# Kernel tuning notes

Hardware: AMD Instinct MI355X
Metric: run time of the kernel (lower is better)

## Reference

```python
import jax, jax.numpy as jnp
import numpy as np
from jax import lax

K = 5        # kernel_size
KN = 32      # kernel_num
C_IN = 16
PRIOR_VAR = 0.01


def _extract_patches(x, k):
    # TF tf.image.extract_patches VALID, stride 1: last-dim order is (kh, kw, c)
    B, H, W, C = x.shape
    Ho, Wo = H - k + 1, W - k + 1
    p = jnp.stack([x[:, i:i + Ho, j:j + Wo, :] for i in range(k) for j in range(k)], axis=3)
    return p.reshape(B, Ho * Wo, k * k * C)  # [B, P, k*k*C]


def setup_inputs() -> dict:
    key = jax.random.key(0)
    k1, k2, k3, k4 = jax.random.split(key, 4)
    mu_in = jax.random.normal(k1, (32, 64, 64, C_IN), dtype=jnp.float32)
    Sigma_in = jax.random.uniform(k2, (32, 64, 64, C_IN), dtype=jnp.float32)
    # GlorotNormal for w_mu
    fan_in = K * K * C_IN
    fan_out = K * K * KN
    std = jnp.sqrt(2.0 / (fan_in + fan_out)).astype(jnp.float32)
    w_mu = jax.random.normal(k3, (K, K, C_IN, KN), dtype=jnp.float32) * std
    w_sigma = jax.random.uniform(k4, (KN,), dtype=jnp.float32, minval=-4.6, maxval=-2.25)
    return {"mu_in": mu_in, "Sigma_in": Sigma_in, "w_mu": w_mu, "w_sigma": w_sigma}


def reference(mu_in, Sigma_in, w_mu, w_sigma):
    B = mu_in.shape[0]
    # KL regularizer (broadcast w_sigma over w_mu shape, mean over all)
    kl_loss = (jnp.log(PRIOR_VAR) - 1.0 - w_sigma
               + jax.nn.softplus(w_sigma) / PRIOR_VAR
               + jnp.square(w_mu) / PRIOR_VAR)
    kl_conv = 0.5 * jnp.mean(kl_loss)

    w_sigma_2 = jax.nn.softplus(w_sigma)  # [KN]

    # mean path: standard conv
    mu_out = lax.conv_general_dilated(
        mu_in, w_mu, window_strides=(1, 1), padding='VALID',
        dimension_numbers=('NHWC', 'HWIO', 'NHWC'))  # [B, Ho, Wo, KN]
    Ho = mu_out.shape[1]

    mu_dim = jnp.float32(K * K * C_IN)

    diag_sigma_g = _extract_patches(Sigma_in, K)          # [B, P, D]
    mu_in_patches = _extract_patches(mu_in, K)            # [B, P, D]

    mu_cov_square = jnp.square(w_mu).reshape(K * K * C_IN, KN)
    mu_wT_sigmags_mu_w = diag_sigma_g @ (mu_cov_square / mu_dim)          # [B, P, KN]
    trace = jnp.sum(diag_sigma_g, axis=2, keepdims=True) * w_sigma_2 / mu_dim  # [B, P, KN]
    mu_gT_mu_g = jnp.sum(jnp.square(mu_in_patches), axis=-1, keepdims=True)    # [B, P, 1]
    sigmaw_mu_gT_mu_g = mu_gT_mu_g * w_sigma_2 / mu_dim                   # [B, P, KN]

    Sigma_out = trace + mu_wT_sigmags_mu_w + sigmaw_mu_gT_mu_g
    Sigma_out = jax.nn.softplus(Sigma_out.reshape(B, Ho, Ho, KN))
    return mu_out, Sigma_out, kl_conv
```

## Files before the change

kernel.cpp:

```cpp
#include <hip/hip_runtime.h>
#include <hip/hip_bf16.h>
#include <math.h>

#define KK 5
#define KN 32
#define CIN 16
#define H 64
#define W 64
#define NB 32
#define HO 60
#define WO 60
#define D_TOT 400
#define OUT_PLANE (NB*HO*WO*KN)

#define TH 8
#define TW 16
#define IN_R 12
#define IN_C 20
#define CPAD 24
#define TILE_SH (IN_R*IN_C*CPAD)
#define NPOS 25

typedef short short8 __attribute__((ext_vector_type(8)));
typedef float f32x16 __attribute__((ext_vector_type(16)));

__device__ ushort g_bmu[NPOS * 64 * 8];
__device__ ushort g_bsq[NPOS * 64 * 8];
__device__ float  g_spw[KN];

__device__ __forceinline__ ushort f2bf(float x) {
    __hip_bfloat16 h = __float2bfloat16(x);
    return *reinterpret_cast<ushort*>(&h);
}
__device__ __forceinline__ float softplusf(float x) {
    return (x > 20.0f) ? x : __logf(1.0f + __expf(x));
}

__global__ void prep_all(const float* __restrict__ w_mu, const float* __restrict__ w_sigma,
                         float* __restrict__ kl_out) {
    __shared__ float red[256];
    int t = threadIdx.x;
    if (blockIdx.x < 50) {
        int idx = blockIdx.x * 256 + t;
        int j  = idx & 7;
        int l  = (idx >> 3) & 63;
        int ts = idx >> 9;
        int cin = ((l >> 5) & 1) * 8 + j;
        int n   = l & 31;
        float w = w_mu[ts * 512 + cin * 32 + n];
        g_bmu[idx] = f2bf(w);
        g_bsq[idx] = f2bf(w * w * (1.0f / 400.0f));
    } else {
        float s = 0.f;
        for (int i = t; i < D_TOT * KN; i += 256) { float w = w_mu[i]; s += w * w; }
        red[t] = s;
        __syncthreads();
        for (int off = 128; off > 0; off >>= 1) {
            if (t < off) red[t] += red[t + off];
            __syncthreads();
        }
        float sum_w2 = red[0];
        if (t < KN) {
            float ws = w_sigma[t];
            g_spw[t] = log1pf(expf(ws)) * (1.0f / 400.0f);
        }
        if (t == 0) {
            float sws = 0.f;
            for (int kn = 0; kn < KN; ++kn) {
                float ws = w_sigma[kn];
                float sp = log1pf(expf(ws));
                sws += -ws + sp * 100.0f;
            }
            float kl = 0.5f * (-4.605170186f - 1.0f + sws * (1.0f / 32.0f)
                               + sum_w2 * (100.0f / 12800.0f));
            *kl_out = kl;
        }
    }
}

__global__ __launch_bounds__(256, 4)
void vdp_main(const float* __restrict__ mu_in, const float* __restrict__ sig_in,
              float* __restrict__ mu_out, float* __restrict__ sig_out) {
    __shared__ ushort tiles[2 * TILE_SH];
    __shared__ float csum[IN_R * IN_C];
    __shared__ float t12s[TH * TW];

    const int b   = blockIdx.z;
    const int ho0 = blockIdx.y * TH;
    const int wo0 = blockIdx.x * TW;
    const int t   = threadIdx.x;

    for (int i = t; i < IN_R * IN_C * 4; i += 256) {
        int pix = i >> 2, c4 = i & 3;
        int row = pix / IN_C;
        int col = pix - row * IN_C;
        int gh = ho0 + row, gw = wo0 + col;
        float4 vm = make_float4(0.f, 0.f, 0.f, 0.f), vs = vm;
        if (gh < H && gw < W) {
            size_t g = (((size_t)b * H + gh) * W + gw) * CIN + c4 * 4;
            vm = *(const float4*)(mu_in + g);
            vs = *(const float4*)(sig_in + g);
        }
        int sb = pix * CPAD + c4 * 4;
        ushort4 um, us;
        um.x = f2bf(vm.x); um.y = f2bf(vm.y); um.z = f2bf(vm.z); um.w = f2bf(vm.w);
        us.x = f2bf(vs.x); us.y = f2bf(vs.y); us.z = f2bf(vs.z); us.w = f2bf(vs.w);
        *(ushort4*)&tiles[sb] = um;
        *(ushort4*)&tiles[TILE_SH + sb] = us;
        float part = vs.x + vs.y + vs.z + vs.w
                   + vm.x * vm.x + vm.y * vm.y + vm.z * vm.z + vm.w * vm.w;
        part += __shfl_down(part, 2, 4);
        part += __shfl_down(part, 1, 4);
        if (c4 == 0) csum[pix] = part;
    }
    __syncthreads();

    if (t < TH * TW) {
        int r = t >> 4, c = t & 15;
        float s = 0.f;
#pragma unroll
        for (int kh = 0; kh < KK; ++kh)
#pragma unroll
            for (int kw = 0; kw < KK; ++kw)
                s += csum[(r + kh) * IN_C + c + kw];
        t12s[t] = s;
    }
    __syncthreads();

    const int w   = t >> 6;
    const int l   = t & 63;
    const int p   = l & 31;
    const int hi  = l >> 5;
    const int pr  = p >> 4;
    const int pc  = p & 15;

    const char* lds = (const char*)tiles;
    const int abase = ((2 * w + pr) * IN_C + pc) * (CPAD * 2) + hi * 16;

    const short8* Bmu8 = (const short8*)g_bmu;
    const short8* Bsq8 = (const short8*)g_bsq;

    f32x16 accm = {0.f}, accs = {0.f};
#pragma unroll
    for (int kh = 0; kh < KK; ++kh) {
#pragma unroll
        for (int kw = 0; kw < KK; ++kw) {
            const int ts  = kh * KK + kw;
            const int off = (kh * IN_C + kw) * (CPAD * 2);
            short8 am = *(const short8*)(lds + abase + off);
            short8 as = *(const short8*)(lds + abase + off + TILE_SH * 2);
            short8 bm = Bmu8[ts * 64 + l];
            short8 bs = Bsq8[ts * 64 + l];
            accm = __builtin_amdgcn_mfma_f32_32x32x16_bf16(am, bm, accm, 0, 0, 0);
            accs = __builtin_amdgcn_mfma_f32_32x32x16_bf16(as, bs, accs, 0, 0, 0);
        }
    }

    const int n = l & 31;
    const float spwn = g_spw[n];
#pragma unroll
    for (int reg = 0; reg < 16; ++reg) {
        int rloc = (reg & 3) + 8 * (reg >> 2) + 4 * hi;
        int lr = rloc >> 4, lc = rloc & 15;
        int ho = ho0 + 2 * w + lr;
        int wo = wo0 + lc;
        if (ho < HO && wo < WO) {
            float t12v = t12s[(2 * w + lr) * TW + lc];
            size_t base = (((size_t)b * HO + ho) * WO + wo) * KN + n;
            mu_out[base]  = accm[reg];
            sig_out[base] = softplusf(accs[reg] + t12v * spwn);
        }
    }
}

extern "C" void kernel_launch(void* const* d_in, const int* in_sizes, int n_in,
                              void* d_out, int out_size, void* d_ws, size_t ws_size,
                              hipStream_t stream) {
    const float* mu_in   = (const float*)d_in[0];
    const float* sig_in  = (const float*)d_in[1];
    const float* w_mu    = (const float*)d_in[2];
    const float* w_sigma = (const float*)d_in[3];

    float* out     = (float*)d_out;
    float* mu_out  = out;
    float* sig_out = out + (size_t)OUT_PLANE;
    float* kl_out  = out + 2 * (size_t)OUT_PLANE;

    (void)d_ws; (void)ws_size;

    prep_all<<<51, 256, 0, stream>>>(w_mu, w_sigma, kl_out);
    vdp_main<<<dim3(4, 8, NB), 256, 0, stream>>>(mu_in, sig_in, mu_out, sig_out);
}
```

Baseline: 114.1 us.

## Fuse weight prep into main kernel using atomic tickets and spin-wait

Merges the weight-preparation kernel into the main conv kernel. The first 26 blocks to draw an atomic ticket build the bf16 weight fragments and the KL term, and every block spin-waits on a done counter before its MFMA loop. The per-channel softplus scale now lives in shared memory. This removes one kernel launch and the gap between launches, at the cost of a global spin barrier and counters that the last block must reset. It relies on the ticketed blocks being resident, and concurrent launches could race on the shared counters.

```diff
diff --git a/kernel.cpp b/kernel.cpp
--- a/kernel.cpp
+++ b/kernel.cpp
@@ -20,13 +20,16 @@
 #define CPAD 24
 #define TILE_SH (IN_R*IN_C*CPAD)
 #define NPOS 25
+#define NBLK (4*8*NB)
 
 typedef short short8 __attribute__((ext_vector_type(8)));
 typedef float f32x16 __attribute__((ext_vector_type(16)));
 
 __device__ ushort g_bmu[NPOS * 64 * 8];
 __device__ ushort g_bsq[NPOS * 64 * 8];
-__device__ float  g_spw[KN];
+__device__ int g_ticket = 0;
+__device__ int g_done   = 0;
+__device__ int g_fin    = 0;
 
 __device__ __forceinline__ ushort f2bf(float x) {
     __hip_bfloat16 h = __float2bfloat16(x);
@@ -36,59 +39,76 @@
     return (x > 20.0f) ? x : __logf(1.0f + __expf(x));
 }
 
-__global__ void prep_all(const float* __restrict__ w_mu, const float* __restrict__ w_sigma,
-                         float* __restrict__ kl_out) {
+__global__ __launch_bounds__(256, 4)
+void vdp_fused(const float* __restrict__ mu_in, const float* __restrict__ sig_in,
+               const float* __restrict__ w_mu, const float* __restrict__ w_sigma,
+               float* __restrict__ mu_out, float* __restrict__ sig_out,
+               float* __restrict__ kl_out) {
+    __shared__ ushort tiles[2 * TILE_SH];
+    __shared__ float csum[IN_R * IN_C];
+    __shared__ float t12s[TH * TW];
+    __shared__ float s_spw[KN];
     __shared__ float red[256];
-    int t = threadIdx.x;
-    if (blockIdx.x < 50) {
-        int idx = blockIdx.x * 256 + t;
-        int j  = idx & 7;
-        int l  = (idx >> 3) & 63;
-        int ts = idx >> 9;
-        int cin = ((l >> 5) & 1) * 8 + j;
-        int n   = l & 31;
-        float w = w_mu[ts * 512 + cin * 32 + n];
-        g_bmu[idx] = f2bf(w);
-        g_bsq[idx] = f2bf(w * w * (1.0f / 400.0f));
-    } else {
+    __shared__ int s_tk;
+
+    const int b   = blockIdx.z;
+    const int ho0 = blockIdx.y * TH;
+    const int wo0 = blockIdx.x * TW;
+    const int t   = threadIdx.x;
+
+    if (t == 0)
+        s_tk = __hip_atomic_fetch_add(&g_ticket, 1, __ATOMIC_RELAXED,
+                                      __HIP_MEMORY_SCOPE_AGENT);
+    __syncthreads();
+    const int tk = s_tk;
+
+    if (tk < NPOS) {
+        if (t < 128) {
+            const int l = t & 63, hi = l >> 5, n = l & 31;
+            const float* wp = w_mu + tk * 512 + hi * 256 + n;
+            float wv[8];
+#pragma unroll
+            for (int j = 0; j < 8; ++j) wv[j] = wp[j * 32];
+            short8 fr;
+            if (t < 64) {
+#pragma unroll
+                for (int j = 0; j < 8; ++j) fr[j] = (short)f2bf(wv[j]);
+                *(short8*)&g_bmu[(tk * 64 + l) * 8] = fr;
+            } else {
+#pragma unroll
+                for (int j = 0; j < 8; ++j)
+                    fr[j] = (short)f2bf(wv[j] * wv[j] * (1.0f / 400.0f));
+                *(short8*)&g_bsq[(tk * 64 + l) * 8] = fr;
+            }
+        }
+        __threadfence();
+        __syncthreads();
+        if (t == 0)
+            __hip_atomic_fetch_add(&g_done, 1, __ATOMIC_RELEASE,
+                                   __HIP_MEMORY_SCOPE_AGENT);
+    } else if (tk == NPOS) {
         float s = 0.f;
-        for (int i = t; i < D_TOT * KN; i += 256) { float w = w_mu[i]; s += w * w; }
+        for (int i = t; i < D_TOT * KN; i += 256) { float wv = w_mu[i]; s += wv * wv; }
         red[t] = s;
         __syncthreads();
         for (int off = 128; off > 0; off >>= 1) {
             if (t < off) red[t] += red[t + off];
             __syncthreads();
         }
-        float sum_w2 = red[0];
-        if (t < KN) {
-            float ws = w_sigma[t];
-            g_spw[t] = log1pf(expf(ws)) * (1.0f / 400.0f);
-        }
         if (t == 0) {
+            float sum_w2 = red[0];
             float sws = 0.f;
             for (int kn = 0; kn < KN; ++kn) {
                 float ws = w_sigma[kn];
                 float sp = log1pf(expf(ws));
                 sws += -ws + sp * 100.0f;
             }
-            float kl = 0.5f * (-4.605170186f - 1.0f + sws * (1.0f / 32.0f)
-                               + sum_w2 * (100.0f / 12800.0f));
-            *kl_out = kl;
-        }
-    }
-}
-
-__global__ __launch_bounds__(256, 4)
-void vdp_main(const float* __restrict__ mu_in, const float* __restrict__ sig_in,
-              float* __restrict__ mu_out, float* __restrict__ sig_out) {
-    __shared__ ushort tiles[2 * TILE_SH];
-    __shared__ float csum[IN_R * IN_C];
-    __shared__ float t12s[TH * TW];
-
-    const int b   = blockIdx.z;
-    const int ho0 = blockIdx.y * TH;
-    const int wo0 = blockIdx.x * TW;
-    const int t   = threadIdx.x;
+            *kl_out = 0.5f * (-4.605170186f - 1.0f + sws * (1.0f / 32.0f)
+                              + sum_w2 * (100.0f / 12800.0f));
+        }
+    }
+
+    if (t < KN) s_spw[t] = log1pf(expf(w_sigma[t])) * (1.0f / 400.0f);
 
     for (int i = t; i < IN_R * IN_C * 4; i += 256) {
         int pix = i >> 2, c4 = i & 3;
@@ -127,6 +147,13 @@
     }
     __syncthreads();
 
+    if (t == 0) {
+        while (__hip_atomic_load(&g_done, __ATOMIC_ACQUIRE,
+                                 __HIP_MEMORY_SCOPE_AGENT) < NPOS)
+            __builtin_amdgcn_s_sleep(2);
+    }
+    __syncthreads();
+
     const int w   = t >> 6;
     const int l   = t & 63;
     const int p   = l & 31;
@@ -157,7 +184,7 @@
     }
 
     const int n = l & 31;
-    const float spwn = g_spw[n];
+    const float spwn = s_spw[n];
 #pragma unroll
     for (int reg = 0; reg < 16; ++reg) {
         int rloc = (reg & 3) + 8 * (reg >> 2) + 4 * hi;
@@ -171,6 +198,17 @@
             sig_out[base] = softplusf(accs[reg] + t12v * spwn);
         }
     }
+
+    __syncthreads();
+    if (t == 0) {
+        int f = __hip_atomic_fetch_add(&g_fin, 1, __ATOMIC_ACQ_REL,
+                                       __HIP_MEMORY_SCOPE_AGENT);
+        if (f == NBLK - 1) {
+            __hip_atomic_store(&g_ticket, 0, __ATOMIC_RELAXED, __HIP_MEMORY_SCOPE_AGENT);
+            __hip_atomic_store(&g_done,   0, __ATOMIC_RELAXED, __HIP_MEMORY_SCOPE_AGENT);
+            __hip_atomic_store(&g_fin,    0, __ATOMIC_RELAXED, __HIP_MEMORY_SCOPE_AGENT);
+        }
+    }
 }
 
 extern "C" void kernel_launch(void* const* d_in, const int* in_sizes, int n_in,
@@ -188,6 +226,6 @@
 
     (void)d_ws; (void)ws_size;
 
-    prep_all<<<51, 256, 0, stream>>>(w_mu, w_sigma, kl_out);
-    vdp_main<<<dim3(4, 8, NB), 256, 0, stream>>>(mu_in, sig_in, mu_out, sig_out);
-}
+    vdp_fused<<<dim3(4, 8, NB), 256, 0, stream>>>(mu_in, sig_in, w_mu, w_sigma,
+                                                  mu_out, sig_out, kl_out);
+}
```

New measurement: 171.4 us. 1.5x slower.
